# Kernel optimization log

Measured on AMD Instinct MI355X. Metric: run time of the kernel, lower is better.

Reference implementation:

```python
import jax, jax.numpy as jnp
import numpy as np

N = 50000      # atoms
P = 1_600_000  # pairs
F = 128        # per-atom features
G = 16         # radial basis functions
H = 32         # vector features
HID1, HID2 = 256, 128
IN_F = 2 * F + 2 * H  # is_first_module=False: [rad_emb, vec_emb, rad_q, vec_q]


def setup_inputs() -> dict:
    key = jax.random.key(0)
    ks = jax.random.split(key, 13)
    return {
        "atomic_embedding": jax.random.normal(ks[0], (N, F), jnp.float32),
        "partial_charges": jax.random.normal(ks[1], (N, 1), jnp.float32),
        "pair_indices": jax.random.randint(ks[2], (2, P), 0, N),
        "gs": jax.random.uniform(ks[3], (P, G), jnp.float32),
        "gv": jax.random.normal(ks[4], (P, 3, G), jnp.float32),
        "agh": jax.random.normal(ks[5], (F, G, H), jnp.float32) * 0.05,
        "W_gf": jax.random.normal(ks[6], (G, F), jnp.float32) * 0.1,   # gs_to_fatom (no bias)
        "W1": jax.random.normal(ks[7], (IN_F, HID1), jnp.float32) * 0.05,
        "b1": jnp.zeros((HID1,), jnp.float32),
        "W2": jax.random.normal(ks[8], (HID1, HID2), jnp.float32) * 0.05,
        "b2": jnp.zeros((HID2,), jnp.float32),
        "W3": jax.random.normal(ks[9], (HID2, F + 2), jnp.float32) * 0.05,
        "b3": jnp.zeros((F + 2,), jnp.float32),
    }


def _safe_norm(x):
    # torch.norm has subgradient 0 at 0; avoid NaN grads for all-zero rows
    sq = jnp.sum(x * x, axis=-1)
    return jnp.sqrt(jnp.where(sq > 0, sq, 1.0)) * (sq > 0)


def _gelu(x):
    return jax.nn.gelu(x, approximate=False)  # torch nn.GELU default (erf)


def reference(atomic_embedding, partial_charges, pair_indices, gs, gv, agh,
              W_gf, W1, b1, W2, b2, W3, b3):
    idx_j = pair_indices[1]                       # (P,)
    a_j = atomic_embedding[idx_j]                 # (P, F) gather
    mapped_gs = gs @ W_gf                         # (P, F)

    # radial contributions from embeddings: scatter-add over pairs
    rad_emb = jnp.zeros((N, F), mapped_gs.dtype).at[idx_j].add(a_j * mapped_gs)

    # vector contributions: einsum contraction then scatter-add, then norm
    avf_v = jnp.einsum('pa,pdg,agh->phd', a_j, gv, agh)            # (P, H, 3)
    avf_sum = jnp.zeros((N, H, 3), avf_v.dtype).at[idx_j].add(avf_v)
    vec_emb = _safe_norm(avf_sum)                                   # (N, H)

    # charge branch (vector contributions skipped -> zeros)
    q_j = partial_charges[idx_j]                                    # (P, 1)
    rad_q = jnp.zeros((N, F), mapped_gs.dtype).at[idx_j].add(q_j * mapped_gs)
    vec_q = jnp.zeros((N, H), mapped_gs.dtype)

    msg = jnp.concatenate([rad_emb, vec_emb, rad_q, vec_q], axis=1)  # (N, IN_F)
    h = _gelu(msg @ W1 + b1)
    h = _gelu(h @ W2 + b2)
    out = h @ W3 + b3                                                # (N, F+2)

    delta_q, f, delta_a = out[:, :1], out[:, 1:2], out[:, 2:]
    return (delta_a, delta_q, f)
```

## Files before the change

### kernel.cpp

```cpp
#include <hip/hip_runtime.h>
#include <math.h>

#define N_ATOMS 50000
#define P_PAIRS 1600000
#define TA 16
#define CAP_MAX 96

__device__ __forceinline__ float gelu_exact(float x) {
    return 0.5f * x * (1.0f + erff(x * 0.70710678118654752440f));
}

__global__ __launch_bounds__(256) void build_buckets(
    const int* __restrict__ idx_j,
    int* __restrict__ cnt,
    int* __restrict__ bucket,
    int cap)
{
    int p = blockIdx.x * 256 + threadIdx.x;
    int idx = idx_j[p];
    int pos = atomicAdd(cnt + idx, 1);
    if (pos < cap) bucket[(size_t)idx * cap + pos] = p;
}

__global__ __launch_bounds__(256, 3) void fused_atom_kernel(
    const float* __restrict__ emb,
    const float* __restrict__ qch,
    const int* __restrict__ cnt,
    const int* __restrict__ bucket,
    const float* __restrict__ gs,
    const float* __restrict__ gv,
    const float* __restrict__ agh,
    const float* __restrict__ W_gf,
    const float* __restrict__ W1, const float* __restrict__ b1,
    const float* __restrict__ W2, const float* __restrict__ b2,
    const float* __restrict__ W3, const float* __restrict__ b3,
    int cap,
    float* __restrict__ out)
{
    __shared__ __align__(16) float s_bufA[16 * 256];
    __shared__ __align__(16) float s_bufB[16 * 512];
    __shared__ __align__(16) float s_gs[16 * 16];
    __shared__ __align__(16) float s_gv[16 * 48];
    __shared__ __align__(16) float s_q[16];

    const int tid = threadIdx.x;
    const int n0 = blockIdx.x * TA;

    float* s_embT = s_bufA;
    float* s_h1T  = s_bufA;
    float* s_U    = s_bufB;
    float* s_msgT = s_bufB;
    float* s_h2T  = s_bufB;

    #pragma unroll
    for (int i = 0; i < 2; i++) {
        int ii = tid + i * 256;
        int atom = ii >> 5;
        int a4 = (ii & 31) * 4;
        float4 v = *(const float4*)(emb + (size_t)(n0 + atom) * 128 + a4);
        s_embT[(a4 + 0) * 16 + atom] = v.x;
        s_embT[(a4 + 1) * 16 + atom] = v.y;
        s_embT[(a4 + 2) * 16 + atom] = v.z;
        s_embT[(a4 + 3) * 16 + atom] = v.w;
    }

    {
        const int g = tid >> 4;
        const int l = tid & 15;
        const int n = n0 + g;
        int c = cnt[n]; if (c > cap) c = cap;
        const int* brow = bucket + (size_t)n * cap;
        const float* base; int stride;
        if (l < 4) { base = gs + l * 4;       stride = 16; }
        else       { base = gv + (l - 4) * 4; stride = 48; }
        float4 a = make_float4(0.f, 0.f, 0.f, 0.f);
        int i = 0;
        for (; i + 4 <= c; i += 4) {
            int p0 = brow[i + 0], p1 = brow[i + 1];
            int p2 = brow[i + 2], p3 = brow[i + 3];
            float4 v0 = *(const float4*)(base + (size_t)p0 * stride);
            float4 v1 = *(const float4*)(base + (size_t)p1 * stride);
            float4 v2 = *(const float4*)(base + (size_t)p2 * stride);
            float4 v3 = *(const float4*)(base + (size_t)p3 * stride);
            a.x += (v0.x + v1.x) + (v2.x + v3.x);
            a.y += (v0.y + v1.y) + (v2.y + v3.y);
            a.z += (v0.z + v1.z) + (v2.z + v3.z);
            a.w += (v0.w + v1.w) + (v2.w + v3.w);
        }
        for (; i < c; i++) {
            int p0 = brow[i];
            float4 v0 = *(const float4*)(base + (size_t)p0 * stride);
            a.x += v0.x; a.y += v0.y; a.z += v0.z; a.w += v0.w;
        }
        if (l < 4) *(float4*)(s_gs + g * 16 + l * 4)       = a;
        else       *(float4*)(s_gv + g * 48 + (l - 4) * 4) = a;
    }
    if (tid < 16) s_q[tid] = qch[n0 + tid];
    __syncthreads();

    {
        const int gh4  = (tid & 127) * 4;
        const int half = tid >> 7;
        float u[32];
        #pragma unroll
        for (int i = 0; i < 32; i++) u[i] = 0.f;
        #pragma unroll 4
        for (int a = 0; a < 128; a++) {
            float4 w  = *(const float4*)(agh + a * 512 + gh4);
            float4 e0 = *(const float4*)(s_embT + a * 16 + half * 8);
            float4 e1 = *(const float4*)(s_embT + a * 16 + half * 8 + 4);
            float wv[4] = {w.x, w.y, w.z, w.w};
            float ev[8] = {e0.x, e0.y, e0.z, e0.w, e1.x, e1.y, e1.z, e1.w};
            #pragma unroll
            for (int j = 0; j < 4; j++)
                #pragma unroll
                for (int m = 0; m < 8; m++)
                    u[j * 8 + m] += wv[j] * ev[m];
        }
        #pragma unroll
        for (int m = 0; m < 8; m++) {
            int atom = half * 8 + m;
            float4 v = {u[0 * 8 + m], u[1 * 8 + m], u[2 * 8 + m], u[3 * 8 + m]};
            *(float4*)(s_U + atom * 512 + gh4) = v;
        }
    }
    __syncthreads();

    float nrm[2];
    #pragma unroll
    for (int it = 0; it < 2; it++) {
        int i = tid + it * 256;
        int atom = i >> 5, h = i & 31;
        float v0 = 0.f, v1 = 0.f, v2 = 0.f;
        #pragma unroll
        for (int g = 0; g < 16; g++) {
            float uv = s_U[atom * 512 + g * 32 + h];
            v0 += uv * s_gv[atom * 48 + g];
            v1 += uv * s_gv[atom * 48 + 16 + g];
            v2 += uv * s_gv[atom * 48 + 32 + g];
        }
        float sq = v0 * v0 + v1 * v1 + v2 * v2;
        nrm[it] = (sq > 0.f) ? sqrtf(sq) : 0.f;
    }
    __syncthreads();

    #pragma unroll
    for (int it = 0; it < 2; it++) {
        int i = tid + it * 256;
        int atom = i >> 5, h = i & 31;
        s_msgT[(128 + h) * 16 + atom] = nrm[it];
        s_msgT[(288 + h) * 16 + atom] = 0.f;
    }

    {
        const int f = tid & 127;
        const int half = tid >> 7;
        float mp[8];
        #pragma unroll
        for (int a = 0; a < 8; a++) mp[a] = 0.f;
        #pragma unroll
        for (int g = 0; g < 16; g++) {
            float w = W_gf[g * 128 + f];
            #pragma unroll
            for (int a = 0; a < 8; a++)
                mp[a] += s_gs[(half * 8 + a) * 16 + g] * w;
        }
        #pragma unroll
        for (int a = 0; a < 8; a++) {
            int atom = half * 8 + a;
            float e = s_embT[f * 16 + atom];
            s_msgT[f * 16 + atom]         = e * mp[a];
            s_msgT[(160 + f) * 16 + atom] = s_q[atom] * mp[a];
        }
    }
    __syncthreads();

    {
        const int o4 = (tid & 63) * 4;
        const int q4 = (tid >> 6) * 4;
        float acc1[16];
        #pragma unroll
        for (int i = 0; i < 16; i++) acc1[i] = 0.f;
        #pragma unroll 4
        for (int k = 0; k < 320; k++) {
            float4 w  = *(const float4*)(W1 + k * 256 + o4);
            float4 mm = *(const float4*)(s_msgT + k * 16 + q4);
            float wv[4] = {w.x, w.y, w.z, w.w};
            float mv[4] = {mm.x, mm.y, mm.z, mm.w};
            #pragma unroll
            for (int j = 0; j < 4; j++)
                #pragma unroll
                for (int m = 0; m < 4; m++)
                    acc1[j * 4 + m] += wv[j] * mv[m];
        }
        #pragma unroll
        for (int j = 0; j < 4; j++) {
            int o = o4 + j;
            float bb = b1[o];
            float4 v;
            v.x = gelu_exact(acc1[j * 4 + 0] + bb);
            v.y = gelu_exact(acc1[j * 4 + 1] + bb);
            v.z = gelu_exact(acc1[j * 4 + 2] + bb);
            v.w = gelu_exact(acc1[j * 4 + 3] + bb);
            *(float4*)(s_h1T + o * 16 + q4) = v;
        }
    }
    __syncthreads();

    {
        const int o4 = (tid & 31) * 4;
        const int a2 = (tid >> 5) * 2;
        float acc2[8];
        #pragma unroll
        for (int i = 0; i < 8; i++) acc2[i] = 0.f;
        #pragma unroll 4
        for (int k = 0; k < 256; k++) {
            float4 w  = *(const float4*)(W2 + k * 128 + o4);
            float2 hh = *(const float2*)(s_h1T + k * 16 + a2);
            float wv[4] = {w.x, w.y, w.z, w.w};
            float hv[2] = {hh.x, hh.y};
            #pragma unroll
            for (int j = 0; j < 4; j++)
                #pragma unroll
                for (int m = 0; m < 2; m++)
                    acc2[j * 2 + m] += wv[j] * hv[m];
        }
        __syncthreads();
        #pragma unroll
        for (int j = 0; j < 4; j++) {
            int o = o4 + j;
            float bb = b2[o];
            float2 v;
            v.x = gelu_exact(acc2[j * 2 + 0] + bb);
            v.y = gelu_exact(acc2[j * 2 + 1] + bb);
            *(float2*)(s_h2T + o * 16 + a2) = v;
        }
    }
    __syncthreads();

    {
        const int o4 = (tid & 31) * 4 + 2;
        const int a2 = (tid >> 5) * 2;
        float acc3[8];
        #pragma unroll
        for (int i = 0; i < 8; i++) acc3[i] = 0.f;
        #pragma unroll 4
        for (int k = 0; k < 128; k++) {
            const float* wp = W3 + k * 130 + o4;
            float2 wa = *(const float2*)(wp);
            float2 wb = *(const float2*)(wp + 2);
            float2 hh = *(const float2*)(s_h2T + k * 16 + a2);
            float wv[4] = {wa.x, wa.y, wb.x, wb.y};
            float hv[2] = {hh.x, hh.y};
            #pragma unroll
            for (int j = 0; j < 4; j++)
                #pragma unroll
                for (int m = 0; m < 2; m++)
                    acc3[j * 2 + m] += wv[j] * hv[m];
        }
        #pragma unroll
        for (int m = 0; m < 2; m++) {
            int n = n0 + a2 + m;
            float4 v;
            v.x = acc3[0 * 2 + m] + b3[o4 + 0];
            v.y = acc3[1 * 2 + m] + b3[o4 + 1];
            v.z = acc3[2 * 2 + m] + b3[o4 + 2];
            v.w = acc3[3 * 2 + m] + b3[o4 + 3];
            *(float4*)(out + (size_t)n * 128 + (o4 - 2)) = v;
        }

        if (tid < 32) {
            int atom = tid >> 1, col = tid & 1;
            float s = 0.f;
            #pragma unroll 4
            for (int k = 0; k < 128; k++)
                s += s_h2T[k * 16 + atom] * W3[k * 130 + col];
            s += b3[col];
            out[(size_t)N_ATOMS * 128 + (size_t)col * N_ATOMS + (n0 + atom)] = s;
        }
    }
}

extern "C" void kernel_launch(void* const* d_in, const int* in_sizes, int n_in,
                              void* d_out, int out_size, void* d_ws, size_t ws_size,
                              hipStream_t stream)
{
    const float* emb  = (const float*)d_in[0];
    const float* qch  = (const float*)d_in[1];
    const int*   pidx = (const int*)d_in[2];
    const float* gs   = (const float*)d_in[3];
    const float* gv   = (const float*)d_in[4];
    const float* agh  = (const float*)d_in[5];
    const float* W_gf = (const float*)d_in[6];
    const float* W1   = (const float*)d_in[7];
    const float* b1   = (const float*)d_in[8];
    const float* W2   = (const float*)d_in[9];
    const float* b2   = (const float*)d_in[10];
    const float* W3   = (const float*)d_in[11];
    const float* b3   = (const float*)d_in[12];

    int* cnt = (int*)d_ws;
    const size_t cnt_off = 256 * 1024;
    int* bucket = (int*)((char*)d_ws + cnt_off);
    size_t avail = (ws_size > cnt_off) ? (ws_size - cnt_off) : 0;
    size_t cap_fit = avail / ((size_t)N_ATOMS * sizeof(int));
    int cap = cap_fit > CAP_MAX ? CAP_MAX : (int)cap_fit;

    hipMemsetAsync(cnt, 0, (size_t)N_ATOMS * sizeof(int), stream);

    build_buckets<<<P_PAIRS / 256, 256, 0, stream>>>(
        pidx + P_PAIRS, cnt, bucket, cap);

    fused_atom_kernel<<<N_ATOMS / TA, 256, 0, stream>>>(
        emb, qch, cnt, bucket, gs, gv, agh, W_gf,
        W1, b1, W2, b2, W3, b3, cap, (float*)d_out);
}
```

Baseline: 1.083 ms.

## Shrink shared memory pool, split agh contraction, pad bucket counters

Shared memory is folded into one smaller pool (about 28KB instead of about 52KB), and the launch bound is raised to 5 blocks per SM. To make this fit, the agh contraction runs in two halves over the G dimension, accumulating the vector components in registers. The message tensor is no longer materialised: the radial terms are formed on the fly inside the W1 loop from mapped gs, embeddings and charges, and the zero vec_q rows are skipped. Bucket counters are padded to a 16-int stride so concurrent atomics land on separate cache lines, at the cost of a larger memset and an extra barrier in the W1 stage.

```diff
diff --git a/kernel.cpp b/kernel.cpp
--- a/kernel.cpp
+++ b/kernel.cpp
@@ -5,6 +5,7 @@
 #define P_PAIRS 1600000
 #define TA 16
 #define CAP_MAX 96
+#define CSTRIDE 16
 
 __device__ __forceinline__ float gelu_exact(float x) {
     return 0.5f * x * (1.0f + erff(x * 0.70710678118654752440f));
@@ -18,11 +19,13 @@
 {
     int p = blockIdx.x * 256 + threadIdx.x;
     int idx = idx_j[p];
-    int pos = atomicAdd(cnt + idx, 1);
+    int pos = atomicAdd(cnt + idx * CSTRIDE, 1);
     if (pos < cap) bucket[(size_t)idx * cap + pos] = p;
 }
 
-__global__ __launch_bounds__(256, 3) void fused_atom_kernel(
+#define POOL_FLOATS 7184
+
+__global__ __launch_bounds__(256, 5) void fused_atom_kernel(
     const float* __restrict__ emb,
     const float* __restrict__ qch,
     const int* __restrict__ cnt,
@@ -37,20 +40,20 @@
     int cap,
     float* __restrict__ out)
 {
-    __shared__ __align__(16) float s_bufA[16 * 256];
-    __shared__ __align__(16) float s_bufB[16 * 512];
-    __shared__ __align__(16) float s_gs[16 * 16];
-    __shared__ __align__(16) float s_gv[16 * 48];
-    __shared__ __align__(16) float s_q[16];
+    __shared__ __align__(16) float sp[POOL_FLOATS];
 
     const int tid = threadIdx.x;
     const int n0 = blockIdx.x * TA;
 
-    float* s_embT = s_bufA;
-    float* s_h1T  = s_bufA;
-    float* s_U    = s_bufB;
-    float* s_msgT = s_bufB;
-    float* s_h2T  = s_bufB;
+    float* s_embT = sp;
+    float* s_gs   = sp + 2048;
+    float* s_gv   = sp + 2304;
+    float* s_q    = sp + 3072;
+    float* s_U    = sp + 3088;
+    float* s_map  = sp + 3088;
+    float* s_vec  = sp + 5136;
+    float* s_h1T  = sp;
+    float* s_h2T  = sp + 4096;
 
     #pragma unroll
     for (int i = 0; i < 2; i++) {
@@ -68,7 +71,7 @@
         const int g = tid >> 4;
         const int l = tid & 15;
         const int n = n0 + g;
-        int c = cnt[n]; if (c > cap) c = cap;
+        int c = cnt[n * CSTRIDE]; if (c > cap) c = cap;
         const int* brow = bucket + (size_t)n * cap;
         const float* base; int stride;
         if (l < 4) { base = gs + l * 4;       stride = 16; }
@@ -98,60 +101,62 @@
     if (tid < 16) s_q[tid] = qch[n0 + tid];
     __syncthreads();
 
-    {
-        const int gh4  = (tid & 127) * 4;
-        const int half = tid >> 7;
-        float u[32];
-        #pragma unroll
-        for (int i = 0; i < 32; i++) u[i] = 0.f;
-        #pragma unroll 4
-        for (int a = 0; a < 128; a++) {
-            float4 w  = *(const float4*)(agh + a * 512 + gh4);
-            float4 e0 = *(const float4*)(s_embT + a * 16 + half * 8);
-            float4 e1 = *(const float4*)(s_embT + a * 16 + half * 8 + 4);
-            float wv[4] = {w.x, w.y, w.z, w.w};
-            float ev[8] = {e0.x, e0.y, e0.z, e0.w, e1.x, e1.y, e1.z, e1.w};
-            #pragma unroll
-            for (int j = 0; j < 4; j++)
-                #pragma unroll
-                for (int m = 0; m < 8; m++)
-                    u[j * 8 + m] += wv[j] * ev[m];
-        }
-        #pragma unroll
-        for (int m = 0; m < 8; m++) {
-            int atom = half * 8 + m;
-            float4 v = {u[0 * 8 + m], u[1 * 8 + m], u[2 * 8 + m], u[3 * 8 + m]};
-            *(float4*)(s_U + atom * 512 + gh4) = v;
-        }
-    }
-    __syncthreads();
-
-    float nrm[2];
+    float av[2][3];
+    #pragma unroll
+    for (int it = 0; it < 2; it++) { av[it][0] = 0.f; av[it][1] = 0.f; av[it][2] = 0.f; }
+
+    #pragma unroll
+    for (int ph = 0; ph < 2; ph++) {
+        {
+            const int ghl4 = (tid & 63) * 4;
+            const int quad = tid >> 6;
+            float u[16];
+            #pragma unroll
+            for (int i = 0; i < 16; i++) u[i] = 0.f;
+            #pragma unroll 4
+            for (int a = 0; a < 128; a++) {
+                float4 w = *(const float4*)(agh + a * 512 + ph * 256 + ghl4);
+                float4 e = *(const float4*)(s_embT + a * 16 + quad * 4);
+                float wv[4] = {w.x, w.y, w.z, w.w};
+                float ev[4] = {e.x, e.y, e.z, e.w};
+                #pragma unroll
+                for (int j = 0; j < 4; j++)
+                    #pragma unroll
+                    for (int m = 0; m < 4; m++)
+                        u[j * 4 + m] += wv[j] * ev[m];
+            }
+            #pragma unroll
+            for (int m = 0; m < 4; m++) {
+                int atom = quad * 4 + m;
+                float4 v = {u[0 * 4 + m], u[1 * 4 + m], u[2 * 4 + m], u[3 * 4 + m]};
+                *(float4*)(s_U + atom * 256 + ghl4) = v;
+            }
+        }
+        __syncthreads();
+
+        #pragma unroll
+        for (int it = 0; it < 2; it++) {
+            int i = tid + it * 256;
+            int atom = i >> 5, h = i & 31;
+            #pragma unroll
+            for (int g = 0; g < 8; g++) {
+                float uv = s_U[atom * 256 + g * 32 + h];
+                int gg = ph * 8 + g;
+                av[it][0] += uv * s_gv[atom * 48 + gg];
+                av[it][1] += uv * s_gv[atom * 48 + 16 + gg];
+                av[it][2] += uv * s_gv[atom * 48 + 32 + gg];
+            }
+        }
+        __syncthreads();
+    }
+
     #pragma unroll
     for (int it = 0; it < 2; it++) {
         int i = tid + it * 256;
         int atom = i >> 5, h = i & 31;
-        float v0 = 0.f, v1 = 0.f, v2 = 0.f;
-        #pragma unroll
-        for (int g = 0; g < 16; g++) {
-            float uv = s_U[atom * 512 + g * 32 + h];
-            v0 += uv * s_gv[atom * 48 + g];
-            v1 += uv * s_gv[atom * 48 + 16 + g];
-            v2 += uv * s_gv[atom * 48 + 32 + g];
-        }
-        float sq = v0 * v0 + v1 * v1 + v2 * v2;
-        nrm[it] = (sq > 0.f) ? sqrtf(sq) : 0.f;
-    }
-    __syncthreads();
-
-    #pragma unroll
-    for (int it = 0; it < 2; it++) {
-        int i = tid + it * 256;
-        int atom = i >> 5, h = i & 31;
-        s_msgT[(128 + h) * 16 + atom] = nrm[it];
-        s_msgT[(288 + h) * 16 + atom] = 0.f;
-    }
-
+        float sq = av[it][0] * av[it][0] + av[it][1] * av[it][1] + av[it][2] * av[it][2];
+        s_vec[h * 16 + atom] = (sq > 0.f) ? sqrtf(sq) : 0.f;
+    }
     {
         const int f = tid & 127;
         const int half = tid >> 7;
@@ -166,12 +171,8 @@
                 mp[a] += s_gs[(half * 8 + a) * 16 + g] * w;
         }
         #pragma unroll
-        for (int a = 0; a < 8; a++) {
-            int atom = half * 8 + a;
-            float e = s_embT[f * 16 + atom];
-            s_msgT[f * 16 + atom]         = e * mp[a];
-            s_msgT[(160 + f) * 16 + atom] = s_q[atom] * mp[a];
-        }
+        for (int a = 0; a < 8; a++)
+            s_map[f * 16 + half * 8 + a] = mp[a];
     }
     __syncthreads();
 
@@ -181,18 +182,37 @@
         float acc1[16];
         #pragma unroll
         for (int i = 0; i < 16; i++) acc1[i] = 0.f;
+        float qv[4] = {s_q[q4 + 0], s_q[q4 + 1], s_q[q4 + 2], s_q[q4 + 3]};
+
+        #pragma unroll 2
+        for (int f = 0; f < 128; f++) {
+            float4 wa = *(const float4*)(W1 + f * 256 + o4);
+            float4 wb = *(const float4*)(W1 + (160 + f) * 256 + o4);
+            float4 mm = *(const float4*)(s_map + f * 16 + q4);
+            float4 ee = *(const float4*)(s_embT + f * 16 + q4);
+            float wav[4] = {wa.x, wa.y, wa.z, wa.w};
+            float wbv[4] = {wb.x, wb.y, wb.z, wb.w};
+            float rm[4]  = {mm.x * ee.x, mm.y * ee.y, mm.z * ee.z, mm.w * ee.w};
+            float rq[4]  = {mm.x * qv[0], mm.y * qv[1], mm.z * qv[2], mm.w * qv[3]};
+            #pragma unroll
+            for (int j = 0; j < 4; j++)
+                #pragma unroll
+                for (int m = 0; m < 4; m++)
+                    acc1[j * 4 + m] += wav[j] * rm[m] + wbv[j] * rq[m];
+        }
         #pragma unroll 4
-        for (int k = 0; k < 320; k++) {
-            float4 w  = *(const float4*)(W1 + k * 256 + o4);
-            float4 mm = *(const float4*)(s_msgT + k * 16 + q4);
+        for (int h = 0; h < 32; h++) {
+            float4 w  = *(const float4*)(W1 + (128 + h) * 256 + o4);
+            float4 vv = *(const float4*)(s_vec + h * 16 + q4);
             float wv[4] = {w.x, w.y, w.z, w.w};
-            float mv[4] = {mm.x, mm.y, mm.z, mm.w};
+            float mv[4] = {vv.x, vv.y, vv.z, vv.w};
             #pragma unroll
             for (int j = 0; j < 4; j++)
                 #pragma unroll
                 for (int m = 0; m < 4; m++)
                     acc1[j * 4 + m] += wv[j] * mv[m];
         }
+        __syncthreads();
         #pragma unroll
         for (int j = 0; j < 4; j++) {
             int o = o4 + j;
@@ -225,7 +245,6 @@
                 for (int m = 0; m < 2; m++)
                     acc2[j * 2 + m] += wv[j] * hv[m];
         }
-        __syncthreads();
         #pragma unroll
         for (int j = 0; j < 4; j++) {
             int o = o4 + j;
@@ -300,13 +319,13 @@
     const float* b3   = (const float*)d_in[12];
 
     int* cnt = (int*)d_ws;
-    const size_t cnt_off = 256 * 1024;
-    int* bucket = (int*)((char*)d_ws + cnt_off);
-    size_t avail = (ws_size > cnt_off) ? (ws_size - cnt_off) : 0;
+    const size_t cnt_bytes = (size_t)N_ATOMS * CSTRIDE * sizeof(int);
+    int* bucket = (int*)((char*)d_ws + cnt_bytes);
+    size_t avail = (ws_size > cnt_bytes) ? (ws_size - cnt_bytes) : 0;
     size_t cap_fit = avail / ((size_t)N_ATOMS * sizeof(int));
     int cap = cap_fit > CAP_MAX ? CAP_MAX : (int)cap_fit;
 
-    hipMemsetAsync(cnt, 0, (size_t)N_ATOMS * sizeof(int), stream);
+    hipMemsetAsync(cnt, 0, cnt_bytes, stream);
 
     build_buckets<<<P_PAIRS / 256, 256, 0, stream>>>(
         pidx + P_PAIRS, cnt, bucket, cap);
```

Result: slower. 1.119 ms (+3.4%).

## Interleave bucket gather of gs/gv with agh contraction to overlap memory latency

Applied to the files above, without the earlier changes.

Moves the per-atom gather-sum of gs/gv rows from its own phase into the agh×embedding contraction loop. Each of 8 chunks issues one group of four gathered float4 loads plus the next bucket-index prefetch, and batches 16 agh rows into registers before the FMAs. The goal is to hide the random-access global load latency behind the FMA work and drop one serialized phase. The cost is higher register pressure (w[16], u[32], gather values) under launch_bounds(256,3), which may cause spills or lower occupancy, plus extra tail-loop code.

```diff
diff --git a/kernel.cpp b/kernel.cpp
--- a/kernel.cpp
+++ b/kernel.cpp
@@ -47,8 +47,8 @@
     const int n0 = blockIdx.x * TA;
 
     float* s_embT = s_bufA;
+    float* s_U    = s_bufB;
     float* s_h1T  = s_bufA;
-    float* s_U    = s_bufB;
     float* s_msgT = s_bufB;
     float* s_h2T  = s_bufB;
 
@@ -63,66 +63,96 @@
         s_embT[(a4 + 2) * 16 + atom] = v.z;
         s_embT[(a4 + 3) * 16 + atom] = v.w;
     }
-
-    {
-        const int g = tid >> 4;
-        const int l = tid & 15;
-        const int n = n0 + g;
-        int c = cnt[n]; if (c > cap) c = cap;
-        const int* brow = bucket + (size_t)n * cap;
-        const float* base; int stride;
-        if (l < 4) { base = gs + l * 4;       stride = 16; }
-        else       { base = gv + (l - 4) * 4; stride = 48; }
-        float4 a = make_float4(0.f, 0.f, 0.f, 0.f);
-        int i = 0;
-        for (; i + 4 <= c; i += 4) {
-            int p0 = brow[i + 0], p1 = brow[i + 1];
-            int p2 = brow[i + 2], p3 = brow[i + 3];
-            float4 v0 = *(const float4*)(base + (size_t)p0 * stride);
-            float4 v1 = *(const float4*)(base + (size_t)p1 * stride);
-            float4 v2 = *(const float4*)(base + (size_t)p2 * stride);
-            float4 v3 = *(const float4*)(base + (size_t)p3 * stride);
-            a.x += (v0.x + v1.x) + (v2.x + v3.x);
-            a.y += (v0.y + v1.y) + (v2.y + v3.y);
-            a.z += (v0.z + v1.z) + (v2.z + v3.z);
-            a.w += (v0.w + v1.w) + (v2.w + v3.w);
-        }
-        for (; i < c; i++) {
-            int p0 = brow[i];
-            float4 v0 = *(const float4*)(base + (size_t)p0 * stride);
-            a.x += v0.x; a.y += v0.y; a.z += v0.z; a.w += v0.w;
-        }
-        if (l < 4) *(float4*)(s_gs + g * 16 + l * 4)       = a;
-        else       *(float4*)(s_gv + g * 48 + (l - 4) * 4) = a;
-    }
     if (tid < 16) s_q[tid] = qch[n0 + tid];
     __syncthreads();
 
     {
         const int gh4  = (tid & 127) * 4;
         const int half = tid >> 7;
+
+        const int ga = tid >> 4;
+        const int gl = tid & 15;
+        int c = cnt[n0 + ga]; if (c > cap) c = cap;
+        const int* brow = bucket + (size_t)(n0 + ga) * cap;
+        const float* gbase; int gstride;
+        if (gl < 4) { gbase = gs + gl * 4;       gstride = 16; }
+        else        { gbase = gv + (gl - 4) * 4; gstride = 48; }
+        float4 gacc = make_float4(0.f, 0.f, 0.f, 0.f);
+        int gi = 0;
+        const int pfmax = (cap >= 4) ? cap - 4 : 0;
+        int4 bq = *(const int4*)(brow);
+
         float u[32];
         #pragma unroll
         for (int i = 0; i < 32; i++) u[i] = 0.f;
-        #pragma unroll 4
-        for (int a = 0; a < 128; a++) {
-            float4 w  = *(const float4*)(agh + a * 512 + gh4);
-            float4 e0 = *(const float4*)(s_embT + a * 16 + half * 8);
-            float4 e1 = *(const float4*)(s_embT + a * 16 + half * 8 + 4);
-            float wv[4] = {w.x, w.y, w.z, w.w};
-            float ev[8] = {e0.x, e0.y, e0.z, e0.w, e1.x, e1.y, e1.z, e1.w};
-            #pragma unroll
-            for (int j = 0; j < 4; j++)
+
+        #pragma unroll 1
+        for (int chunk = 0; chunk < 8; chunk++) {
+            float4 w[16];
+            #pragma unroll
+            for (int aa = 0; aa < 16; aa++)
+                w[aa] = *(const float4*)(agh + (chunk * 16 + aa) * 512 + gh4);
+
+            int pf = gi + 4; if (pf > pfmax) pf = pfmax;
+            int4 bq_next = *(const int4*)(brow + pf);
+
+            float4 g0, g1, g2, g3;
+            const bool have = (gi + 4 <= c);
+            if (have) {
+                g0 = *(const float4*)(gbase + (size_t)bq.x * gstride);
+                g1 = *(const float4*)(gbase + (size_t)bq.y * gstride);
+                g2 = *(const float4*)(gbase + (size_t)bq.z * gstride);
+                g3 = *(const float4*)(gbase + (size_t)bq.w * gstride);
+            }
+
+            #pragma unroll
+            for (int aa = 0; aa < 16; aa++) {
+                int a = chunk * 16 + aa;
+                float4 e0 = *(const float4*)(s_embT + a * 16 + half * 8);
+                float4 e1 = *(const float4*)(s_embT + a * 16 + half * 8 + 4);
+                float wv[4] = {w[aa].x, w[aa].y, w[aa].z, w[aa].w};
+                float ev[8] = {e0.x, e0.y, e0.z, e0.w, e1.x, e1.y, e1.z, e1.w};
                 #pragma unroll
-                for (int m = 0; m < 8; m++)
-                    u[j * 8 + m] += wv[j] * ev[m];
-        }
+                for (int j = 0; j < 4; j++)
+                    #pragma unroll
+                    for (int m = 0; m < 8; m++)
+                        u[j * 8 + m] += wv[j] * ev[m];
+            }
+
+            if (have) {
+                gacc.x += (g0.x + g1.x) + (g2.x + g3.x);
+                gacc.y += (g0.y + g1.y) + (g2.y + g3.y);
+                gacc.z += (g0.z + g1.z) + (g2.z + g3.z);
+                gacc.w += (g0.w + g1.w) + (g2.w + g3.w);
+                gi += 4;
+            }
+            bq = bq_next;
+        }
+
+        for (; gi + 4 <= c; gi += 4) {
+            int p0 = brow[gi], p1 = brow[gi + 1], p2 = brow[gi + 2], p3 = brow[gi + 3];
+            float4 v0 = *(const float4*)(gbase + (size_t)p0 * gstride);
+            float4 v1 = *(const float4*)(gbase + (size_t)p1 * gstride);
+            float4 v2 = *(const float4*)(gbase + (size_t)p2 * gstride);
+            float4 v3 = *(const float4*)(gbase + (size_t)p3 * gstride);
+            gacc.x += (v0.x + v1.x) + (v2.x + v3.x);
+            gacc.y += (v0.y + v1.y) + (v2.y + v3.y);
+            gacc.z += (v0.z + v1.z) + (v2.z + v3.z);
+            gacc.w += (v0.w + v1.w) + (v2.w + v3.w);
+        }
+        for (; gi < c; gi++) {
+            float4 v0 = *(const float4*)(gbase + (size_t)brow[gi] * gstride);
+            gacc.x += v0.x; gacc.y += v0.y; gacc.z += v0.z; gacc.w += v0.w;
+        }
+
         #pragma unroll
         for (int m = 0; m < 8; m++) {
             int atom = half * 8 + m;
             float4 v = {u[0 * 8 + m], u[1 * 8 + m], u[2 * 8 + m], u[3 * 8 + m]};
             *(float4*)(s_U + atom * 512 + gh4) = v;
         }
+        if (gl < 4) *(float4*)(s_gs + ga * 16 + gl * 4)       = gacc;
+        else        *(float4*)(s_gv + ga * 48 + (gl - 4) * 4) = gacc;
     }
     __syncthreads();
 
```

Result: slower. 2.106 ms (+94.5%).
